# Kernel optimization log

Measured on AMD Instinct MI355X. Metric: run time of the kernel, lower is better.

Reference implementation:

```python
import math
import jax, jax.numpy as jnp
import numpy as np

NUM_HEADS = 16
HEAD_DIM = 64
NB_FEATURES = 256
EPS = 1e-06
DATA_NORM = HEAD_DIM ** (-0.25)


def setup_inputs() -> dict:
    key = jax.random.key(0)
    ks = jax.random.split(key, 5)
    B, N, C = 4, 4096, 1024
    x = jax.random.normal(ks[0], (B, N, C), dtype=jnp.float32)
    w_qkv = jax.random.normal(ks[1], (C, 3 * C), dtype=jnp.float32) * (C ** -0.5)
    b_qkv = jnp.zeros((3 * C,), dtype=jnp.float32)
    w_out = jax.random.normal(ks[2], (C, C), dtype=jnp.float32) * (C ** -0.5)
    b_out = jnp.zeros((C,), dtype=jnp.float32)
    proj = jax.random.normal(ks[3], (NUM_HEADS, NB_FEATURES, HEAD_DIM), dtype=jnp.float32)
    proj = proj / jnp.linalg.norm(proj, axis=-1, keepdims=True)  # F.normalize(dim=-1)
    return {"x": x, "w_qkv": w_qkv, "b_qkv": b_qkv, "w_out": w_out, "b_out": b_out,
            "proj_matrix": proj}


def _feature_map(x, proj):
    # x: [b,h,n,d], proj: [h,m,d] -> [b,h,n,m]
    x = x * DATA_NORM
    x_proj = jnp.einsum('bhnd,hmd->bhnm', x, proj)
    sq_norms = 0.5 * jnp.sum(x * x, axis=-1, keepdims=True)
    x_proj = x_proj - sq_norms
    x_proj = x_proj - jnp.max(x_proj, axis=-1, keepdims=True)
    return (jnp.exp(x_proj) + EPS) / math.sqrt(NB_FEATURES)


def reference(x, w_qkv, b_qkv, w_out, b_out, proj_matrix):
    B, N, C = x.shape
    h, d = NUM_HEADS, HEAD_DIM
    qkv = x @ w_qkv + b_qkv                     # [B,N,3C]
    q, k, v = jnp.split(qkv, 3, axis=-1)
    to_heads = lambda z: z.reshape(B, N, h, d).transpose(0, 2, 1, 3)  # [B,h,N,d]
    q, k, v = to_heads(q), to_heads(k), to_heads(v)

    q_prime = _feature_map(q, proj_matrix)      # [B,h,N,m]
    k_prime = _feature_map(k, proj_matrix)      # [B,h,N,m]

    k_sum = jnp.sum(k_prime, axis=2)                          # [B,h,m]
    kv = jnp.einsum('bhnm,bhnd->bhmd', k_prime, v)            # [B,h,m,d]
    numerator = jnp.einsum('bhnm,bhmd->bhnd', q_prime, kv)    # [B,h,N,d]
    denominator = jnp.einsum('bhnm,bhm->bhn', q_prime, k_sum) + EPS
    out = numerator / denominator[..., None]

    out = out.transpose(0, 2, 1, 3).reshape(B, N, C)
    return out @ w_out + b_out
```

## Files before the change

### kernel.cpp

```cpp
#include <hip/hip_runtime.h>
#include <hip/hip_bf16.h>
#include <stdint.h>


#define DN 0.35355339059327379f
#define EPSF 1e-6f
#define INV_SQRT_M 0.0625f

typedef __attribute__((ext_vector_type(8))) short bf16x8;
typedef __attribute__((ext_vector_type(4))) float f32x4;

static __device__ __forceinline__ short f2bf(float f) {
    __hip_bfloat16 h = __float2bfloat16(f);
    return *(short*)&h;
}
static __device__ __forceinline__ void gload16(const void* g, void* l) {
    __builtin_amdgcn_global_load_lds(
        (const __attribute__((address_space(1))) void*)g,
        (__attribute__((address_space(3))) void*)l,
        16, 0, 0);
}

__global__ __launch_bounds__(256) void conv_x(const float* __restrict__ X,
                                              short* __restrict__ Xb) {
    int i = blockIdx.x * 256 + threadIdx.x;
    float4 v = ((const float4*)X)[i];
    short4 o;
    o.x = f2bf(v.x); o.y = f2bf(v.y); o.z = f2bf(v.z); o.w = f2bf(v.w);
    ((short4*)Xb)[i] = o;
}

__global__ __launch_bounds__(256) void convt_w(const float* __restrict__ W,
                                               short* __restrict__ WT,
                                               int K, int NN) {
    __shared__ short tile[64][66];
    int t = threadIdx.x;
    int k0 = blockIdx.y * 64, n0 = blockIdx.x * 64;
    for (int i = t; i < 4096; i += 256) {
        int r = i >> 6, c = i & 63;
        tile[r][c] = f2bf(W[(size_t)(k0 + r) * NN + n0 + c]);
    }
    __syncthreads();
    for (int i = t; i < 4096; i += 256) {
        int r = i >> 6, c = i & 63;
        WT[(size_t)(n0 + r) * K + k0 + c] = tile[c][r];
    }
}

__global__ __launch_bounds__(256) void conv_proj(const float* __restrict__ proj,
                                                 short* __restrict__ pjb) {
    int e = blockIdx.x * 256 + threadIdx.x;
    int m = (e >> 6) & 255, d = e & 63;
    int base = e & ~63;
    pjb[base + (d ^ ((m & 7) << 3))] = f2bf(proj[e]);
}

template<int Q, int S>
static __device__ __forceinline__ void phase_compute(
        const char* smem, int tt, int wm, int wn, int li, int g, int swz,
        f32x4 (&acc)[2][4][2][2]) {
    const char* bA = smem + ((tt & 1) << 16) + (Q << 14);
    const char* bB = smem + ((tt & 1) << 16) + 32768 + (S << 14);
    bf16x8 af[4][2], bf[2][2];
#pragma unroll
    for (int fr = 0; fr < 4; ++fr) {
        int row = wm * 64 + fr * 16 + li;
#pragma unroll
        for (int kk = 0; kk < 2; ++kk)
            af[fr][kk] = *(const bf16x8*)(bA + row * 128 + ((kk * 64 + g * 16) ^ swz));
    }
#pragma unroll
    for (int fn = 0; fn < 2; ++fn) {
        int row = wn * 32 + fn * 16 + li;
#pragma unroll
        for (int kk = 0; kk < 2; ++kk)
            bf[fn][kk] = *(const bf16x8*)(bB + row * 128 + ((kk * 64 + g * 16) ^ swz));
    }
    __builtin_amdgcn_s_setprio(1);
#pragma unroll
    for (int kk = 0; kk < 2; ++kk)
#pragma unroll
        for (int fr = 0; fr < 4; ++fr)
#pragma unroll
            for (int fn = 0; fn < 2; ++fn)
                acc[Q][fr][S][fn] = __builtin_amdgcn_mfma_f32_16x16x32_bf16(
                    af[fr][kk], bf[fn][kk], acc[Q][fr][S][fn], 0, 0, 0);
    __builtin_amdgcn_s_setprio(0);
}

static __device__ __forceinline__ void gemm_core256(const short* __restrict__ A,
                                                    const short* __restrict__ BT,
                                                    int rowBase, int colBase,
                                                    char* smem,
                                                    f32x4 (&acc)[2][4][2][2]) {
    const int K = 1024;
    int t = threadIdx.x, lane = t & 63;
    int li = lane & 15, g = lane >> 4;
    int w = t >> 6, wm = w >> 2, wn = w & 3;
    int swz = (li & 7) << 4;

    int idxA = t, idxB = 512 + t;
    int rA = idxA >> 3, sA = idxA & 7;
    int rB = idxB >> 3, sB = idxB & 7;
    const char* Ab = (const char*)(A + (size_t)rowBase * K);
    const char* Bb = (const char*)(BT + (size_t)colBase * K);
    int srcOffA = rA * 2048 + ((sA ^ (rA & 7)) * 16);
    int srcOffB = rB * 2048 + ((sB ^ (rB & 7)) * 16);
    int dstOffA = idxA * 16, dstOffB = idxB * 16;

#define STG(op_, half_, tile_) do {                                           \
    char* d_ = smem + (((tile_) & 1) << 16) + ((op_) << 15) + ((half_) << 14);\
    const char* s_ = ((op_) ? Bb : Ab) + (half_) * 262144 + (tile_) * 128;    \
    gload16(s_ + srcOffA, d_ + dstOffA);                                      \
    gload16(s_ + srcOffB, d_ + dstOffB);                                      \
} while (0)

#define PH(q_, s_, vm_, dost_, sop_, shalf_, stile_) do {                     \
    if (dost_) STG(sop_, shalf_, stile_);                                     \
    asm volatile("s_waitcnt vmcnt(" #vm_ ")" ::: "memory");                   \
    __builtin_amdgcn_sched_barrier(0);                                        \
    __builtin_amdgcn_s_barrier();                                             \
    __builtin_amdgcn_sched_barrier(0);                                        \
    phase_compute<q_, s_>(smem, tt, wm, wn, li, g, swz, acc);                 \
} while (0)

#pragma unroll
    for (int q = 0; q < 2; ++q)
#pragma unroll
        for (int fr = 0; fr < 4; ++fr)
#pragma unroll
            for (int s = 0; s < 2; ++s)
#pragma unroll
                for (int fn = 0; fn < 2; ++fn)
                    acc[q][fr][s][fn] = (f32x4){0.f, 0.f, 0.f, 0.f};

    STG(1, 0, 0);
    STG(0, 1, 0);
    STG(0, 0, 0);
    STG(1, 1, 0);
    STG(1, 0, 1);
    STG(0, 1, 1);

    for (int tt = 0; tt < 14; ++tt) {
        PH(0, 0,  8, true, 0, 0, tt + 1);
        PH(1, 0, 12, true, 1, 1, tt + 1);
        PH(1, 1, 10, true, 1, 0, tt + 2);
        PH(0, 1, 12, true, 0, 1, tt + 2);
    }
    {
        int tt = 14;
        PH(0, 0,  8, true, 0, 0, 15);
        PH(1, 0, 12, true, 1, 1, 15);
        PH(1, 1,  8, false, 0, 0, 0);
        PH(0, 1,  8, false, 0, 0, 0);
    }
    {
        int tt = 15;
        PH(0, 0, 2, false, 0, 0, 0);
        PH(1, 0, 4, false, 0, 0, 0);
        PH(1, 1, 0, false, 0, 0, 0);
        PH(0, 1, 0, false, 0, 0, 0);
    }
    __builtin_amdgcn_s_barrier();
#undef PH
#undef STG
}

__global__ __launch_bounds__(512) void mfma_gemm_qkv(
        const short* __restrict__ A, const short* __restrict__ BT,
        const float* __restrict__ bias,
        short* __restrict__ Qh, short* __restrict__ Kh, short* __restrict__ Vt) {
    __shared__ __align__(16) char smem[131072];
    int lin = blockIdx.x;
    int bx = lin % 12, by = lin / 12;
    int rowBase = by * 256, colBase = bx * 256;

    f32x4 acc[2][4][2][2];
    gemm_core256(A, BT, rowBase, colBase, smem, acc);

    int t = threadIdx.x, lane = t & 63, w = t >> 6;
    int li = lane & 15, g = lane >> 4, wm = w >> 2, wn = w & 3;
    float bcol[2][2];
#pragma unroll
    for (int s = 0; s < 2; ++s)
#pragma unroll
        for (int fn = 0; fn < 2; ++fn)
            bcol[s][fn] = bias[colBase + s * 128 + wn * 32 + fn * 16 + li];
    int whichB = colBase >> 10;

    if (whichB == 2) {
#pragma unroll
        for (int s = 0; s < 2; ++s)
#pragma unroll
            for (int fn = 0; fn < 2; ++fn) {
                int dd = (wn & 1) * 32 + fn * 16 + li;
                int hh = ((colBase & 1023) >> 6) + s * 2 + (wn >> 1);
#pragma unroll
                for (int q = 0; q < 2; ++q)
#pragma unroll
                    for (int fr = 0; fr < 4; ++fr) {
                        int gr0 = rowBase + q * 128 + wm * 64 + fr * 16 + g * 4;
                        int b = gr0 >> 12, nn0 = gr0 & 4095;
                        short4 o;
                        o.x = f2bf(acc[q][fr][s][fn][0] + bcol[s][fn]);
                        o.y = f2bf(acc[q][fr][s][fn][1] + bcol[s][fn]);
                        o.z = f2bf(acc[q][fr][s][fn][2] + bcol[s][fn]);
                        o.w = f2bf(acc[q][fr][s][fn][3] + bcol[s][fn]);
                        int nsw = (nn0 & ~63) | ((nn0 & 63) ^ ((dd & 7) << 3));
                        *(short4*)&Vt[((size_t)(b * 16 + hh) * 64 + dd) * 4096 + nsw] = o;
                    }
            }
    } else {
        short* dst = (whichB == 0) ? Qh : Kh;
        float* wreg = (float*)(smem + w * 5120);
#pragma unroll
        for (int q = 0; q < 2; ++q)
#pragma unroll
            for (int fp = 0; fp < 2; ++fp)
#pragma unroll
                for (int s = 0; s < 2; ++s) {
                    int hh = ((colBase & 1023) >> 6) + s * 2 + (wn >> 1);
#pragma unroll
                    for (int fr2 = 0; fr2 < 2; ++fr2)
#pragma unroll
                        for (int fn = 0; fn < 2; ++fn)
#pragma unroll
                            for (int jj = 0; jj < 4; ++jj)
                                wreg[(fr2 * 16 + g * 4 + jj) * 40 + fn * 16 + li] =
                                    (acc[q][fp * 2 + fr2][s][fn][jj] + bcol[s][fn]) * DN;
                    int row2 = lane >> 1, hh2 = lane & 1;
                    int tok = rowBase + q * 128 + wm * 64 + fp * 32 + row2;
                    int b = tok >> 12, nn = tok & 4095;
                    size_t base = ((size_t)(b * 16 + hh) * 4096 + nn) * 64;
#pragma unroll
                    for (int k = 0; k < 2; ++k) {
                        float4 v0 = *(const float4*)&wreg[row2 * 40 + hh2 * 16 + k * 8];
                        float4 v1 = *(const float4*)&wreg[row2 * 40 + hh2 * 16 + k * 8 + 4];
                        bf16x8 ov;
                        ov[0] = f2bf(v0.x); ov[1] = f2bf(v0.y);
                        ov[2] = f2bf(v0.z); ov[3] = f2bf(v0.w);
                        ov[4] = f2bf(v1.x); ov[5] = f2bf(v1.y);
                        ov[6] = f2bf(v1.z); ov[7] = f2bf(v1.w);
                        int dgrp = ((wn & 1) * 4 + hh2 * 2 + k) ^ (tok & 7);
                        *(bf16x8*)&dst[base + dgrp * 8] = ov;
                    }
                }
    }
}

__global__ __launch_bounds__(512) void mfma_gemm_out(
        const short* __restrict__ A, const short* __restrict__ BT,
        const float* __restrict__ bias, float* __restrict__ C) {
    __shared__ __align__(16) char smem[131072];
    int lin = blockIdx.x;
    int bx = lin & 3, by = lin >> 2;
    int rowBase = by * 256, colBase = bx * 256;

    f32x4 acc[2][4][2][2];
    gemm_core256(A, BT, rowBase, colBase, smem, acc);

    int t = threadIdx.x, lane = t & 63, w = t >> 6;
    int li = lane & 15, g = lane >> 4, wm = w >> 2, wn = w & 3;
    float bcol[2][2];
#pragma unroll
    for (int s = 0; s < 2; ++s)
#pragma unroll
        for (int fn = 0; fn < 2; ++fn)
            bcol[s][fn] = bias[colBase + s * 128 + wn * 32 + fn * 16 + li];

    float* wreg = (float*)(smem + w * 5120);
#pragma unroll
    for (int q = 0; q < 2; ++q)
#pragma unroll
        for (int fp = 0; fp < 2; ++fp)
#pragma unroll
            for (int s = 0; s < 2; ++s) {
#pragma unroll
                for (int fr2 = 0; fr2 < 2; ++fr2)
#pragma unroll
                    for (int fn = 0; fn < 2; ++fn)
#pragma unroll
                        for (int jj = 0; jj < 4; ++jj)
                            wreg[(fr2 * 16 + g * 4 + jj) * 40 + fn * 16 + li] =
                                acc[q][fp * 2 + fr2][s][fn][jj] + bcol[s][fn];
                int row2 = lane >> 1, hh2 = lane & 1;
                int gr = rowBase + q * 128 + wm * 64 + fp * 32 + row2;
                float* cp = C + (size_t)gr * 1024 + colBase + s * 128 + wn * 32 + hh2 * 16;
#pragma unroll
                for (int k = 0; k < 4; ++k)
                    *(float4*)&cp[k * 4] = *(const float4*)&wreg[row2 * 40 + hh2 * 16 + k * 4];
            }
}

__global__ __launch_bounds__(256) void fmap_mfma(const short* __restrict__ Kh,
                                                 const short* __restrict__ Vt,
                                                 const short* __restrict__ pjb,
                                                 float* __restrict__ kvpart,
                                                 float* __restrict__ kspart) {
    int bh = blockIdx.y, ch = blockIdx.x, h = bh & 15;
    int t = threadIdx.x, lane = t & 63, w = t >> 6;
    int g = lane >> 4, li = lane & 15;
    __shared__ __align__(16) short pj[256 * 64];
    __shared__ __align__(16) short kt[64 * 64];
    __shared__ __align__(16) short vt[64 * 64];
    __shared__ __align__(16) short Pl[4][64 * 40];
    __shared__ __align__(16) float maxw[4][64];

    const short* kbase = Kh + ((size_t)bh * 4096 + ch * 512) * 64;
    const short* vbase = Vt + (size_t)bh * 64 * 4096 + ch * 512;

    {
        const short* psrc = pjb + (size_t)h * 16384;
#pragma unroll
        for (int c2 = 0; c2 < 8; ++c2) {
            int c = 8 * w + c2;
            gload16(psrc + c * 512 + lane * 8, pj + c * 512);
        }
#pragma unroll
        for (int c2 = 0; c2 < 2; ++c2) {
            int c = 2 * w + c2;
            gload16(kbase + c * 512 + lane * 8, kt + c * 512);
            int d = 8 * c + (lane >> 3);
            gload16(vbase + (size_t)d * 4096 + (lane & 7) * 8, vt + c * 512);
        }
    }
    __syncthreads();

    f32x4 acc[4][4];
#pragma unroll
    for (int i = 0; i < 4; ++i)
#pragma unroll
        for (int j = 0; j < 4; ++j) acc[i][j] = (f32x4){0.f, 0.f, 0.f, 0.f};
    float ksacc[4] = {0.f, 0.f, 0.f, 0.f};

    int swz = (li & 7) << 4;

    for (int tile = 0; tile < 8; ++tile) {
        bf16x8 rk0, rk1, rv0, rv1;
        if (tile < 7) {
            int c0 = 2 * w, c1 = 2 * w + 1;
            size_t kof = (size_t)((tile + 1) * 64) * 64;
            rk0 = *(const bf16x8*)(kbase + kof + c0 * 512 + lane * 8);
            rk1 = *(const bf16x8*)(kbase + kof + c1 * 512 + lane * 8);
            int d0 = 8 * c0 + (lane >> 3), d1 = 8 * c1 + (lane >> 3);
            rv0 = *(const bf16x8*)(vbase + (size_t)d0 * 4096 + (tile + 1) * 64 + (lane & 7) * 8);
            rv1 = *(const bf16x8*)(vbase + (size_t)d1 * 4096 + (tile + 1) * 64 + (lane & 7) * 8);
        }

        f32x4 sacc[4][4];
#pragma unroll
        for (int i = 0; i < 4; ++i)
#pragma unroll
            for (int j = 0; j < 4; ++j) sacc[i][j] = (f32x4){0.f, 0.f, 0.f, 0.f};
#pragma unroll
        for (int ks = 0; ks < 2; ++ks) {
            int kb = ks * 64 + g * 16;
            bf16x8 afr[4], bfr[4];
#pragma unroll
            for (int ni = 0; ni < 4; ++ni)
                afr[ni] = *(const bf16x8*)((const char*)kt +
                           (16 * ni + li) * 128 + (kb ^ swz));
#pragma unroll
            for (int mi = 0; mi < 4; ++mi)
                bfr[mi] = *(const bf16x8*)((const char*)pj +
                           (64 * w + 16 * mi + li) * 128 + (kb ^ swz));
#pragma unroll
            for (int ni = 0; ni < 4; ++ni)
#pragma unroll
                for (int mi = 0; mi < 4; ++mi)
                    sacc[ni][mi] = __builtin_amdgcn_mfma_f32_16x16x32_bf16(
                        afr[ni], bfr[mi], sacc[ni][mi], 0, 0, 0);
        }

        float mxl[4][4];
#pragma unroll
        for (int ni = 0; ni < 4; ++ni)
#pragma unroll
            for (int jj = 0; jj < 4; ++jj) {
                float m0 = fmaxf(sacc[ni][0][jj], sacc[ni][1][jj]);
                float m1 = fmaxf(sacc[ni][2][jj], sacc[ni][3][jj]);
                mxl[ni][jj] = fmaxf(m0, m1);
            }
#pragma unroll
        for (int off = 1; off <= 8; off <<= 1)
#pragma unroll
            for (int ni = 0; ni < 4; ++ni)
#pragma unroll
                for (int jj = 0; jj < 4; ++jj)
                    mxl[ni][jj] = fmaxf(mxl[ni][jj], __shfl_xor(mxl[ni][jj], off));
        if (li == 0) {
#pragma unroll
            for (int ni = 0; ni < 4; ++ni)
                *(float4*)&maxw[w][16 * ni + 4 * g] =
                    make_float4(mxl[ni][0], mxl[ni][1], mxl[ni][2], mxl[ni][3]);
        }
        __syncthreads();

#pragma unroll
        for (int hf = 0; hf < 2; ++hf) {
#pragma unroll
            for (int ni2 = 0; ni2 < 2; ++ni2) {
                int ni = 2 * hf + ni2;
                float4 a0 = *(const float4*)&maxw[0][16 * ni + 4 * g];
                float4 a1 = *(const float4*)&maxw[1][16 * ni + 4 * g];
                float4 a2 = *(const float4*)&maxw[2][16 * ni + 4 * g];
                float4 a3 = *(const float4*)&maxw[3][16 * ni + 4 * g];
                float mm[4];
                mm[0] = fmaxf(fmaxf(a0.x, a1.x), fmaxf(a2.x, a3.x));
                mm[1] = fmaxf(fmaxf(a0.y, a1.y), fmaxf(a2.y, a3.y));
                mm[2] = fmaxf(fmaxf(a0.z, a1.z), fmaxf(a2.z, a3.z));
                mm[3] = fmaxf(fmaxf(a0.w, a1.w), fmaxf(a2.w, a3.w));
#pragma unroll
                for (int mi = 0; mi < 4; ++mi) {
                    float p0 = (__expf(sacc[ni][mi][0] - mm[0]) + EPSF) * INV_SQRT_M;
                    float p1 = (__expf(sacc[ni][mi][1] - mm[1]) + EPSF) * INV_SQRT_M;
                    float p2 = (__expf(sacc[ni][mi][2] - mm[2]) + EPSF) * INV_SQRT_M;
                    float p3 = (__expf(sacc[ni][mi][3] - mm[3]) + EPSF) * INV_SQRT_M;
                    ksacc[mi] += (p0 + p1) + (p2 + p3);
                    uint32_t u0 = (uint32_t)(uint16_t)f2bf(p0) |
                                  ((uint32_t)(uint16_t)f2bf(p1) << 16);
                    uint32_t u1 = (uint32_t)(uint16_t)f2bf(p2) |
                                  ((uint32_t)(uint16_t)f2bf(p3) << 16);
                    int m_l = 16 * mi + li;
                    *(uint2*)((char*)Pl[w] + m_l * 80 + 32 * ni2 + 8 * g) =
                        make_uint2(u0, u1);
                }
            }
#pragma unroll
            for (int mi = 0; mi < 4; ++mi) {
                bf16x8 pa = *(const bf16x8*)((const char*)Pl[w] +
                             (16 * mi + li) * 80 + 16 * g);
#pragma unroll
                for (int di = 0; di < 4; ++di) {
                    bf16x8 bv = *(const bf16x8*)((const char*)vt +
                                 (16 * di + li) * 128 + ((64 * hf + 16 * g) ^ swz));
                    acc[mi][di] = __builtin_amdgcn_mfma_f32_16x16x32_bf16(
                        pa, bv, acc[mi][di], 0, 0, 0);
                }
            }
        }
        __syncthreads();
        if (tile < 7) {
            int c0 = 2 * w, c1 = 2 * w + 1;
            *(bf16x8*)((char*)kt + c0 * 1024 + lane * 16) = rk0;
            *(bf16x8*)((char*)kt + c1 * 1024 + lane * 16) = rk1;
            *(bf16x8*)((char*)vt + c0 * 1024 + lane * 16) = rv0;
            *(bf16x8*)((char*)vt + c1 * 1024 + lane * 16) = rv1;
            __syncthreads();
        }
    }

#pragma unroll
    for (int mi = 0; mi < 4; ++mi) {
        ksacc[mi] += __shfl_xor(ksacc[mi], 16);
        ksacc[mi] += __shfl_xor(ksacc[mi], 32);
    }
    if (lane < 16) {
#pragma unroll
        for (int mi = 0; mi < 4; ++mi)
            kspart[(bh * 8 + ch) * 256 + 64 * w + 16 * mi + li] = ksacc[mi];
    }
    float* kvb = kvpart + (size_t)(bh * 8 + ch) * 16384;
#pragma unroll
    for (int mi = 0; mi < 4; ++mi)
#pragma unroll
        for (int di = 0; di < 4; ++di) {
            int d = 16 * di + li, m0 = 64 * w + 16 * mi + 4 * g;
            *(float4*)&kvb[d * 256 + m0] =
                make_float4(acc[mi][di][0], acc[mi][di][1],
                            acc[mi][di][2], acc[mi][di][3]);
        }
}

__global__ __launch_bounds__(256) void reduce_kv(const float* __restrict__ kvpart,
                                                 const float* __restrict__ kspart,
                                                 short* __restrict__ kvsT) {
    int bh = blockIdx.y, bx = blockIdx.x, t = threadIdx.x;
    if (bx < 4) {
#pragma unroll
        for (int i = 0; i < 16; ++i) {
            int idx = t + i * 256;
            int d = 16 * bx + (idx >> 8), m = idx & 255;
            float s = 0.f;
            size_t base = ((size_t)(bh * 8) * 64 + d) * 256 + m;
#pragma unroll
            for (int c = 0; c < 8; ++c) s += kvpart[base + (size_t)c * 16384];
            int widx = (m & 128) + ((m & 127) ^ ((d & 7) << 3));
            kvsT[((size_t)bh * 80 + d) * 256 + widx] = f2bf(s);
        }
    } else {
        float s = 0.f;
#pragma unroll
        for (int c = 0; c < 8; ++c) s += kspart[((bh * 8 + c) << 8) + t];
        kvsT[((size_t)bh * 80 + 64) * 256 + t] = f2bf(s);
        for (int i = t; i < 15 * 256; i += 256) {
            int r = 65 + (i >> 8), cc = i & 255;
            kvsT[((size_t)bh * 80 + r) * 256 + cc] = 0;
        }
    }
}

__global__ __launch_bounds__(256) void contract_mfma(
        const short* __restrict__ Qh,
        const short* __restrict__ pjb,
        const short* __restrict__ kvsT,
        short* __restrict__ attn) {
    int bh = blockIdx.y, rb = blockIdx.x, h = bh & 15, b = bh >> 4;
    int t = threadIdx.x, lane = t & 63, w = t >> 6;
    __shared__ __align__(16) short qs[128 * 64];
    __shared__ __align__(16) short pj[128 * 64];
    __shared__ __align__(16) short Pl[64 * 128];
    __shared__ __align__(16) short kvl[80 * 128];

    {
        const short* src = Qh + ((size_t)bh * 4096 + rb * 128) * 64;
#pragma unroll
        for (int c2 = 0; c2 < 4; ++c2) {
            int c = 4 * w + c2;
            gload16(src + (c * 8 + (lane >> 3)) * 64 + (lane & 7) * 8,
                    qs + c * 512);
        }
    }

    f32x4 acc5[2][5];
#pragma unroll
    for (int rg = 0; rg < 2; ++rg)
#pragma unroll
        for (int i = 0; i < 5; ++i) acc5[rg][i] = (f32x4){0.f, 0.f, 0.f, 0.f};

    int g = lane >> 4, li = lane & 15;

    for (int half = 0; half < 2; ++half) {
        const short* psrc = pjb + (size_t)h * 16384 + half * 8192;
#pragma unroll
        for (int c2 = 0; c2 < 4; ++c2) {
            int c = 4 * w + c2;
            gload16(psrc + (c * 8 + (lane >> 3)) * 64 + (lane & 7) * 8,
                    pj + c * 512);
        }
        const short* ksrc = kvsT + (size_t)bh * 80 * 256 + half * 128;
#pragma unroll
        for (int c2 = 0; c2 < 5; ++c2) {
            int c = 5 * w + c2;
            gload16(ksrc + (c * 4 + (lane >> 4)) * 256 + (lane & 15) * 8,
                    kvl + c * 512);
        }
        __syncthreads();

#pragma unroll
        for (int rg = 0; rg < 2; ++rg) {
            f32x4 sacc[2][4];
#pragma unroll
            for (int mi = 0; mi < 2; ++mi)
#pragma unroll
                for (int ni = 0; ni < 4; ++ni) sacc[mi][ni] = (f32x4){0.f, 0.f, 0.f, 0.f};
#pragma unroll
            for (int ks = 0; ks < 2; ++ks) {
                int kbyte = ks * 64 + g * 16;
                bf16x8 afr[2], bfr[4];
#pragma unroll
                for (int mi = 0; mi < 2; ++mi) {
                    int mr = 32 * w + 16 * mi + li;
                    afr[mi] = *(const bf16x8*)((const char*)pj +
                               mr * 128 + (kbyte ^ ((mr & 7) << 4)));
                }
#pragma unroll
                for (int ni = 0; ni < 4; ++ni) {
                    int qr = rg * 64 + 16 * ni + li;
                    bfr[ni] = *(const bf16x8*)((const char*)qs +
                               qr * 128 + (kbyte ^ ((qr & 7) << 4)));
                }
#pragma unroll
                for (int mi = 0; mi < 2; ++mi)
#pragma unroll
                    for (int ni = 0; ni < 4; ++ni)
                        sacc[mi][ni] = __builtin_amdgcn_mfma_f32_16x16x32_bf16(
                            afr[mi], bfr[ni], sacc[mi][ni], 0, 0, 0);
            }

#pragma unroll
            for (int mi = 0; mi < 2; ++mi) {
                int m0 = 32 * w + 16 * mi + 4 * g;
#pragma unroll
                for (int ni = 0; ni < 4; ++ni) {
                    int row = 16 * ni + li;
                    float e0 = (__expf(sacc[mi][ni][0]) + EPSF) * INV_SQRT_M;
                    float e1 = (__expf(sacc[mi][ni][1]) + EPSF) * INV_SQRT_M;
                    float e2 = (__expf(sacc[mi][ni][2]) + EPSF) * INV_SQRT_M;
                    float e3 = (__expf(sacc[mi][ni][3]) + EPSF) * INV_SQRT_M;
                    uint32_t u0 = (uint32_t)(uint16_t)f2bf(e0) |
                                  ((uint32_t)(uint16_t)f2bf(e1) << 16);
                    uint32_t u1 = (uint32_t)(uint16_t)f2bf(e2) |
                                  ((uint32_t)(uint16_t)f2bf(e3) << 16);
                    int byte = row * 256 + ((m0 * 2) ^ ((row & 7) << 4));
                    *(uint2*)((char*)Pl + byte) = make_uint2(u0, u1);
                }
            }
            __syncthreads();

            int rowA = 16 * w + li;
            int abase = rowA * 256;
            int asw = (rowA & 7) << 4;
#pragma unroll
            for (int ks = 0; ks < 4; ++ks) {
                int kbyte = ks * 64 + g * 16;
                bf16x8 pa = *(const bf16x8*)((const char*)Pl + abase + (kbyte ^ asw));
#pragma unroll
                for (int ni = 0; ni < 5; ++ni) {
                    int rowB = 16 * ni + li;
                    bf16x8 bv = *(const bf16x8*)((const char*)kvl +
                                 rowB * 256 + (kbyte ^ ((rowB & 7) << 4)));
                    acc5[rg][ni] = __builtin_amdgcn_mfma_f32_16x16x32_bf16(
                        pa, bv, acc5[rg][ni], 0, 0, 0);
                }
            }
            __syncthreads();
        }
    }

#pragma unroll
    for (int rg = 0; rg < 2; ++rg) {
        float dj[4];
#pragma unroll
        for (int jj = 0; jj < 4; ++jj)
            dj[jj] = __shfl(acc5[rg][4][jj], lane & 48) + EPSF;
#pragma unroll
        for (int ni = 0; ni < 4; ++ni) {
            int d = 16 * ni + li;
#pragma unroll
            for (int jj = 0; jj < 4; ++jj) {
                int n = rb * 128 + rg * 64 + 16 * w + 4 * g + jj;
                attn[((size_t)b * 4096 + n) * 1024 + h * 64 + d] =
                    f2bf(acc5[rg][ni][jj] / dj[jj]);
            }
        }
    }
}

extern "C" void kernel_launch(void* const* d_in, const int* in_sizes, int n_in,
                              void* d_out, int out_size, void* d_ws, size_t ws_size,
                              hipStream_t stream) {
    const float* x      = (const float*)d_in[0];
    const float* w_qkv  = (const float*)d_in[1];
    const float* b_qkv  = (const float*)d_in[2];
    const float* w_out  = (const float*)d_in[3];
    const float* b_out  = (const float*)d_in[4];
    const float* proj   = (const float*)d_in[5];
    float* out = (float*)d_out;

    char* w = (char*)d_ws;
    short* xb     = (short*)(w);
    short* wqT    = (short*)(w + 33554432);
    short* wOT    = (short*)(w + 39845888);
    short* Qh     = (short*)(w + 41943040);
    short* Kh     = (short*)(w + 75497472);
    short* Vt     = (short*)(w + 109051904);
    float* kvpart = (float*)(w);
    float* kspart = (float*)(w + 142606336);
    short* kvsT   = (short*)(w + 143130624);
    short* pjb    = (short*)(w + 145752064);
    short* attn   = Kh;

    conv_x<<<dim3(16384), 256, 0, stream>>>(x, xb);
    convt_w<<<dim3(48, 16), 256, 0, stream>>>(w_qkv, wqT, 1024, 3072);
    convt_w<<<dim3(16, 16), 256, 0, stream>>>(w_out, wOT, 1024, 1024);
    conv_proj<<<dim3(1024), 256, 0, stream>>>(proj, pjb);
    mfma_gemm_qkv<<<dim3(768), 512, 0, stream>>>(xb, wqT, b_qkv, Qh, Kh, Vt);
    fmap_mfma<<<dim3(8, 64), 256, 0, stream>>>(Kh, Vt, pjb, kvpart, kspart);
    reduce_kv<<<dim3(5, 64), 256, 0, stream>>>(kvpart, kspart, kvsT);
    contract_mfma<<<dim3(32, 64), 256, 0, stream>>>(Qh, pjb, kvsT, attn);
    mfma_gemm_out<<<dim3(256), 512, 0, stream>>>(attn, wOT, b_out, out);
}
```

Measured before the change: 311.9 us.

## Retile QKV GEMM to 128x128 blocks with double-buffered LDS core

Replaces the 256x256, 512-thread QKV projection GEMM with a new 128x128 tile core using 256 threads, two blocks per CU and a simple double-buffered global-to-LDS pipeline. The aim is better occupancy and load balance across the 3072 resulting tiles. This gives up some operand reuse per tile. It also pads the output GEMM's LDS staging stride to reduce bank conflicts and adds s_setprio around MFMA bursts in the feature-map kernel.

```diff
diff --git a/kernel.cpp b/kernel.cpp
--- a/kernel.cpp
+++ b/kernel.cpp
@@ -53,6 +53,151 @@
     int m = (e >> 6) & 255, d = e & 63;
     int base = e & ~63;
     pjb[base + (d ^ ((m & 7) << 3))] = f2bf(proj[e]);
+}
+
+__device__ __forceinline__ void gemm_core128(const short* __restrict__ A,
+                                             const short* __restrict__ BT,
+                                             int rowBase, int colBase,
+                                             char* smem, f32x4 acc[4][4]) {
+    const int K = 1024;
+    int t = threadIdx.x, lane = t & 63, w = t >> 6;
+    int li = lane & 15, g = lane >> 4;
+    int wm = w >> 1, wn = w & 1;
+
+    const char* aSrc[4]; const char* bSrc[4]; int aOff[4];
+#pragma unroll
+    for (int c = 0; c < 4; ++c) {
+        int idx = c * 256 + t;
+        int r = idx >> 3, s = t & 7;
+        aOff[c] = idx * 16;
+        aSrc[c] = (const char*)(A + (size_t)(rowBase + r) * K + ((s ^ (r & 7)) * 8));
+        bSrc[c] = (const char*)(BT + (size_t)(colBase + r) * K + ((s ^ (r & 7)) * 8));
+    }
+#pragma unroll
+    for (int m = 0; m < 4; ++m)
+#pragma unroll
+        for (int n = 0; n < 4; ++n) acc[m][n] = (f32x4){0.f, 0.f, 0.f, 0.f};
+
+#pragma unroll
+    for (int c = 0; c < 4; ++c) {
+        gload16(aSrc[c], smem + aOff[c]);
+        gload16(bSrc[c], smem + 16384 + aOff[c]);
+    }
+
+    int swz = (li & 7) << 4;
+
+    for (int tt = 0; tt < 16; ++tt) {
+        int cur = tt & 1;
+        if (tt < 15) {
+            char* d = smem + (cur ^ 1) * 32768;
+#pragma unroll
+            for (int c = 0; c < 4; ++c) {
+                gload16(aSrc[c] + (size_t)(tt + 1) * 128, d + aOff[c]);
+                gload16(bSrc[c] + (size_t)(tt + 1) * 128, d + 16384 + aOff[c]);
+            }
+            asm volatile("s_waitcnt vmcnt(8)" ::: "memory");
+        } else {
+            asm volatile("s_waitcnt vmcnt(0)" ::: "memory");
+        }
+        __builtin_amdgcn_sched_barrier(0);
+        __builtin_amdgcn_s_barrier();
+        __builtin_amdgcn_sched_barrier(0);
+        __builtin_amdgcn_s_setprio(1);
+        const char* bA = smem + cur * 32768;
+        const char* bB = bA + 16384;
+#pragma unroll
+        for (int ks = 0; ks < 2; ++ks) {
+            int kb = ks * 64 + g * 16;
+            bf16x8 af[4], bv[4];
+#pragma unroll
+            for (int m = 0; m < 4; ++m)
+                af[m] = *(const bf16x8*)(bA + (wm * 64 + m * 16 + li) * 128 + (kb ^ swz));
+#pragma unroll
+            for (int n = 0; n < 4; ++n)
+                bv[n] = *(const bf16x8*)(bB + (wn * 64 + n * 16 + li) * 128 + (kb ^ swz));
+#pragma unroll
+            for (int m = 0; m < 4; ++m)
+#pragma unroll
+                for (int n = 0; n < 4; ++n)
+                    acc[m][n] = __builtin_amdgcn_mfma_f32_16x16x32_bf16(
+                        af[m], bv[n], acc[m][n], 0, 0, 0);
+        }
+        __builtin_amdgcn_s_setprio(0);
+        __builtin_amdgcn_sched_barrier(0);
+        __builtin_amdgcn_s_barrier();
+        __builtin_amdgcn_sched_barrier(0);
+    }
+}
+
+__global__ __launch_bounds__(256, 2) void mfma_gemm_qkv(
+        const short* __restrict__ A, const short* __restrict__ BT,
+        const float* __restrict__ bias,
+        short* __restrict__ Qh, short* __restrict__ Kh, short* __restrict__ Vt) {
+    __shared__ __align__(16) char smem[65536];
+    int t = threadIdx.x, lane = t & 63, w = t >> 6;
+    int li = lane & 15, g = lane >> 4, wm = w >> 1, wn = w & 1;
+    int lin = blockIdx.x;
+    int bx = lin % 24, by = lin / 24;
+    int rowBase = by * 128, colBase = bx * 128;
+
+    f32x4 acc[4][4];
+    gemm_core128(A, BT, rowBase, colBase, smem, acc);
+
+    float bcol[4];
+#pragma unroll
+    for (int n = 0; n < 4; ++n) bcol[n] = bias[colBase + wn * 64 + n * 16 + li];
+    int whichB = colBase >> 10;
+
+    if (whichB == 2) {
+#pragma unroll
+        for (int n = 0; n < 4; ++n) {
+            int gc = colBase + wn * 64 + n * 16 + li;
+            int hh = (gc & 1023) >> 6, dd = gc & 63;
+#pragma unroll
+            for (int m = 0; m < 4; ++m) {
+                int gr0 = rowBase + wm * 64 + m * 16 + g * 4;
+                int b = gr0 >> 12, nn0 = gr0 & 4095;
+                short4 o;
+                o.x = f2bf(acc[m][n][0] + bcol[n]);
+                o.y = f2bf(acc[m][n][1] + bcol[n]);
+                o.z = f2bf(acc[m][n][2] + bcol[n]);
+                o.w = f2bf(acc[m][n][3] + bcol[n]);
+                int nsw = (nn0 & ~63) | ((nn0 & 63) ^ ((dd & 7) << 3));
+                *(short4*)&Vt[((size_t)(b * 16 + hh) * 64 + dd) * 4096 + nsw] = o;
+            }
+        }
+    } else {
+        short* dst = (whichB == 0) ? Qh : Kh;
+        int hh = ((colBase + wn * 64) & 1023) >> 6;
+        float* wreg = (float*)(smem + w * 8704);
+#pragma unroll
+        for (int r = 0; r < 2; ++r) {
+#pragma unroll
+            for (int mi = 0; mi < 2; ++mi)
+#pragma unroll
+                for (int n = 0; n < 4; ++n)
+#pragma unroll
+                    for (int jj = 0; jj < 4; ++jj)
+                        wreg[(mi * 16 + g * 4 + jj) * 68 + n * 16 + li] =
+                            (acc[2 * r + mi][n][jj] + bcol[n]) * DN;
+            int row = lane >> 1, h2 = lane & 1;
+            int tok = rowBase + wm * 64 + r * 32 + row;
+            int b = tok >> 12, nn = tok & 4095;
+            size_t base = ((size_t)(b * 16 + hh) * 4096 + nn) * 64;
+#pragma unroll
+            for (int k = 0; k < 4; ++k) {
+                float4 v0 = *(const float4*)&wreg[row * 68 + h2 * 32 + k * 8];
+                float4 v1 = *(const float4*)&wreg[row * 68 + h2 * 32 + k * 8 + 4];
+                bf16x8 ov;
+                ov[0] = f2bf(v0.x); ov[1] = f2bf(v0.y);
+                ov[2] = f2bf(v0.z); ov[3] = f2bf(v0.w);
+                ov[4] = f2bf(v1.x); ov[5] = f2bf(v1.y);
+                ov[6] = f2bf(v1.z); ov[7] = f2bf(v1.w);
+                int dgrp = (h2 * 4 + k) ^ (tok & 7);
+                *(bf16x8*)&dst[base + dgrp * 8] = ov;
+            }
+        }
+    }
 }
 
 template<int Q, int S>
@@ -166,88 +311,6 @@
 #undef STG
 }
 
-__global__ __launch_bounds__(512) void mfma_gemm_qkv(
-        const short* __restrict__ A, const short* __restrict__ BT,
-        const float* __restrict__ bias,
-        short* __restrict__ Qh, short* __restrict__ Kh, short* __restrict__ Vt) {
-    __shared__ __align__(16) char smem[131072];
-    int lin = blockIdx.x;
-    int bx = lin % 12, by = lin / 12;
-    int rowBase = by * 256, colBase = bx * 256;
-
-    f32x4 acc[2][4][2][2];
-    gemm_core256(A, BT, rowBase, colBase, smem, acc);
-
-    int t = threadIdx.x, lane = t & 63, w = t >> 6;
-    int li = lane & 15, g = lane >> 4, wm = w >> 2, wn = w & 3;
-    float bcol[2][2];
-#pragma unroll
-    for (int s = 0; s < 2; ++s)
-#pragma unroll
-        for (int fn = 0; fn < 2; ++fn)
-            bcol[s][fn] = bias[colBase + s * 128 + wn * 32 + fn * 16 + li];
-    int whichB = colBase >> 10;
-
-    if (whichB == 2) {
-#pragma unroll
-        for (int s = 0; s < 2; ++s)
-#pragma unroll
-            for (int fn = 0; fn < 2; ++fn) {
-                int dd = (wn & 1) * 32 + fn * 16 + li;
-                int hh = ((colBase & 1023) >> 6) + s * 2 + (wn >> 1);
-#pragma unroll
-                for (int q = 0; q < 2; ++q)
-#pragma unroll
-                    for (int fr = 0; fr < 4; ++fr) {
-                        int gr0 = rowBase + q * 128 + wm * 64 + fr * 16 + g * 4;
-                        int b = gr0 >> 12, nn0 = gr0 & 4095;
-                        short4 o;
-                        o.x = f2bf(acc[q][fr][s][fn][0] + bcol[s][fn]);
-                        o.y = f2bf(acc[q][fr][s][fn][1] + bcol[s][fn]);
-                        o.z = f2bf(acc[q][fr][s][fn][2] + bcol[s][fn]);
-                        o.w = f2bf(acc[q][fr][s][fn][3] + bcol[s][fn]);
-                        int nsw = (nn0 & ~63) | ((nn0 & 63) ^ ((dd & 7) << 3));
-                        *(short4*)&Vt[((size_t)(b * 16 + hh) * 64 + dd) * 4096 + nsw] = o;
-                    }
-            }
-    } else {
-        short* dst = (whichB == 0) ? Qh : Kh;
-        float* wreg = (float*)(smem + w * 5120);
-#pragma unroll
-        for (int q = 0; q < 2; ++q)
-#pragma unroll
-            for (int fp = 0; fp < 2; ++fp)
-#pragma unroll
-                for (int s = 0; s < 2; ++s) {
-                    int hh = ((colBase & 1023) >> 6) + s * 2 + (wn >> 1);
-#pragma unroll
-                    for (int fr2 = 0; fr2 < 2; ++fr2)
-#pragma unroll
-                        for (int fn = 0; fn < 2; ++fn)
-#pragma unroll
-                            for (int jj = 0; jj < 4; ++jj)
-                                wreg[(fr2 * 16 + g * 4 + jj) * 40 + fn * 16 + li] =
-                                    (acc[q][fp * 2 + fr2][s][fn][jj] + bcol[s][fn]) * DN;
-                    int row2 = lane >> 1, hh2 = lane & 1;
-                    int tok = rowBase + q * 128 + wm * 64 + fp * 32 + row2;
-                    int b = tok >> 12, nn = tok & 4095;
-                    size_t base = ((size_t)(b * 16 + hh) * 4096 + nn) * 64;
-#pragma unroll
-                    for (int k = 0; k < 2; ++k) {
-                        float4 v0 = *(const float4*)&wreg[row2 * 40 + hh2 * 16 + k * 8];
-                        float4 v1 = *(const float4*)&wreg[row2 * 40 + hh2 * 16 + k * 8 + 4];
-                        bf16x8 ov;
-                        ov[0] = f2bf(v0.x); ov[1] = f2bf(v0.y);
-                        ov[2] = f2bf(v0.z); ov[3] = f2bf(v0.w);
-                        ov[4] = f2bf(v1.x); ov[5] = f2bf(v1.y);
-                        ov[6] = f2bf(v1.z); ov[7] = f2bf(v1.w);
-                        int dgrp = ((wn & 1) * 4 + hh2 * 2 + k) ^ (tok & 7);
-                        *(bf16x8*)&dst[base + dgrp * 8] = ov;
-                    }
-                }
-    }
-}
-
 __global__ __launch_bounds__(512) void mfma_gemm_out(
         const short* __restrict__ A, const short* __restrict__ BT,
         const float* __restrict__ bias, float* __restrict__ C) {
@@ -268,7 +331,7 @@
         for (int fn = 0; fn < 2; ++fn)
             bcol[s][fn] = bias[colBase + s * 128 + wn * 32 + fn * 16 + li];
 
-    float* wreg = (float*)(smem + w * 5120);
+    float* wreg = (float*)(smem + w * 5632);
 #pragma unroll
     for (int q = 0; q < 2; ++q)
 #pragma unroll
@@ -281,14 +344,14 @@
                     for (int fn = 0; fn < 2; ++fn)
 #pragma unroll
                         for (int jj = 0; jj < 4; ++jj)
-                            wreg[(fr2 * 16 + g * 4 + jj) * 40 + fn * 16 + li] =
+                            wreg[(fr2 * 16 + g * 4 + jj) * 44 + fn * 16 + li] =
                                 acc[q][fp * 2 + fr2][s][fn][jj] + bcol[s][fn];
                 int row2 = lane >> 1, hh2 = lane & 1;
                 int gr = rowBase + q * 128 + wm * 64 + fp * 32 + row2;
                 float* cp = C + (size_t)gr * 1024 + colBase + s * 128 + wn * 32 + hh2 * 16;
 #pragma unroll
                 for (int k = 0; k < 4; ++k)
-                    *(float4*)&cp[k * 4] = *(const float4*)&wreg[row2 * 40 + hh2 * 16 + k * 4];
+                    *(float4*)&cp[k * 4] = *(const float4*)&wreg[row2 * 44 + hh2 * 16 + k * 4];
             }
 }
 
@@ -364,12 +427,14 @@
             for (int mi = 0; mi < 4; ++mi)
                 bfr[mi] = *(const bf16x8*)((const char*)pj +
                            (64 * w + 16 * mi + li) * 128 + (kb ^ swz));
+            __builtin_amdgcn_s_setprio(1);
 #pragma unroll
             for (int ni = 0; ni < 4; ++ni)
 #pragma unroll
                 for (int mi = 0; mi < 4; ++mi)
                     sacc[ni][mi] = __builtin_amdgcn_mfma_f32_16x16x32_bf16(
                         afr[ni], bfr[mi], sacc[ni][mi], 0, 0, 0);
+            __builtin_amdgcn_s_setprio(0);
         }
 
         float mxl[4][4];
@@ -430,6 +495,7 @@
             for (int mi = 0; mi < 4; ++mi) {
                 bf16x8 pa = *(const bf16x8*)((const char*)Pl[w] +
                              (16 * mi + li) * 80 + 16 * g);
+                __builtin_amdgcn_s_setprio(1);
 #pragma unroll
                 for (int di = 0; di < 4; ++di) {
                     bf16x8 bv = *(const bf16x8*)((const char*)vt +
@@ -437,6 +503,7 @@
                     acc[mi][di] = __builtin_amdgcn_mfma_f32_16x16x32_bf16(
                         pa, bv, acc[mi][di], 0, 0, 0);
                 }
+                __builtin_amdgcn_s_setprio(0);
             }
         }
         __syncthreads();
@@ -665,7 +732,7 @@
     convt_w<<<dim3(48, 16), 256, 0, stream>>>(w_qkv, wqT, 1024, 3072);
     convt_w<<<dim3(16, 16), 256, 0, stream>>>(w_out, wOT, 1024, 1024);
     conv_proj<<<dim3(1024), 256, 0, stream>>>(proj, pjb);
-    mfma_gemm_qkv<<<dim3(768), 512, 0, stream>>>(xb, wqT, b_qkv, Qh, Kh, Vt);
+    mfma_gemm_qkv<<<dim3(3072), 256, 0, stream>>>(xb, wqT, b_qkv, Qh, Kh, Vt);
     fmap_mfma<<<dim3(8, 64), 256, 0, stream>>>(Kh, Vt, pjb, kvpart, kspart);
     reduce_kv<<<dim3(5, 64), 256, 0, stream>>>(kvpart, kspart, kvsT);
     contract_mfma<<<dim3(32, 64), 256, 0, stream>>>(Qh, pjb, kvsT, attn);
```

After: 313.1 us. No clear change (+0.4%).
